# Optimization experiments

Measured on AMD Instinct MI355X. Metric: run time of the kernel, lower is better.

## Reference

```python
import jax, jax.numpy as jnp
import numpy as np
from itertools import combinations

NUM_FIELDS = 32
EMB = 64
# static pair index lists for combinations(range(NUM_FIELDS), 2)
_PAIRS = np.array(list(combinations(range(NUM_FIELDS), 2)), dtype=np.int32)  # (496, 2)
I_IDX = jnp.asarray(_PAIRS[:, 0])
J_IDX = jnp.asarray(_PAIRS[:, 1])


def bilinear_each(feats, W):
    # feats: (B, F, E); W: (F-1, E, E) with torch Linear convention y = x @ W[i].T
    # transform fields 0..F-2 with their own weight
    t = jnp.einsum('bfe,foe->bfo', feats[:, :NUM_FIELDS - 1, :], W)  # (B, F-1, E)
    # pair (i, j): t[:, i] * feats[:, j]
    return t[:, I_IDX, :] * feats[:, J_IDX, :]  # (B, P, E)


def se_block(x, se_w1, se_w2):
    # x: (B, F, E)
    Z = jnp.mean(x, axis=-1)                      # (B, F)
    A = jax.nn.relu(Z @ se_w1.T)                  # (B, F//r)
    A = jax.nn.sigmoid(A @ se_w2.T)               # (B, F)
    return x * A[:, :, None]


def setup_inputs() -> dict:
    key = jax.random.key(0)
    ks = jax.random.split(key, 12)
    B, F, E = 1024, NUM_FIELDS, EMB
    P = F * (F - 1) // 2
    d_in = 2 * P * E  # 63488
    h1, h2, nc = 1024, 512, 1
    red = max(1, F // 8)
    s = lambda *sh: 1.0 / np.sqrt(sh[-1])
    inp = {
        'x': jax.random.normal(ks[0], (B, F, E), dtype=jnp.float32),
        'W_bil1': jax.random.normal(ks[1], (F - 1, E, E), jnp.float32) * s(E),
        'W_bil2': jax.random.normal(ks[2], (F - 1, E, E), jnp.float32) * s(E),
        'se_w1': jax.random.normal(ks[3], (red, F), jnp.float32) * s(F),
        'se_w2': jax.random.normal(ks[4], (F, red), jnp.float32) * s(red),
        'fc0_w': jax.random.normal(ks[5], (h1, d_in), jnp.float32) * s(d_in),
        'fc0_b': jnp.zeros((h1,), jnp.float32),
        'fc1_w': jax.random.normal(ks[6], (h2, h1), jnp.float32) * s(h1),
        'fc1_b': jnp.zeros((h2,), jnp.float32),
        'fc2_w': jax.random.normal(ks[7], (nc, h2), jnp.float32) * s(h2),
        'fc2_b': jnp.zeros((nc,), jnp.float32),
    }
    return inp


def reference(x, W_bil1, W_bil2, se_w1, se_w2, fc0_w, fc0_b, fc1_w, fc1_b, fc2_w, fc2_b):
    f1 = bilinear_each(x, W_bil1)                    # (B, P, E)
    f2 = bilinear_each(se_block(x, se_w1, se_w2), W_bil2)  # (B, P, E)
    feat = jnp.concatenate([f1, f2], axis=1).reshape(x.shape[0], -1)  # (B, 2*P*E)
    h = jax.nn.relu(feat @ fc0_w.T + fc0_b)
    h = jax.nn.relu(h @ fc1_w.T + fc1_b)
    y = jax.nn.sigmoid(h @ fc2_w.T + fc2_b)
    return y
```

## Files before the change

kernel.cpp:

```cpp
#include <hip/hip_runtime.h>
#include <hip/hip_bf16.h>
#include <stdint.h>


typedef __attribute__((ext_vector_type(4))) int   int4v;
typedef __attribute__((ext_vector_type(4))) unsigned uint4v;
typedef __attribute__((ext_vector_type(4))) float f32x4;

__device__ __forceinline__ unsigned short f32_bf16(float f) {
  unsigned u = __builtin_bit_cast(unsigned, f);
  u = (u + 0x7fffu + ((u >> 16) & 1u)) >> 16;
  return (unsigned short)u;
}
__device__ __forceinline__ unsigned pk_bf16(float lo, float hi) {
  return (unsigned)f32_bf16(lo) | ((unsigned)f32_bf16(hi) << 16);
}
__device__ __forceinline__ unsigned cvt_pk(float lo, float hi) {
  unsigned r;
  asm("v_cvt_pk_bf16_f32 %0, %1, %2" : "=v"(r) : "v"(lo), "v"(hi));
  return r;
}

__global__ __launch_bounds__(256) void se_kernel(
    const float* __restrict__ x, const float* __restrict__ w1,
    const float* __restrict__ w2, float* __restrict__ scale) {
  __shared__ float Z[32];
  __shared__ float A1[4];
  int b = blockIdx.x;
  int t = threadIdx.x;
  int f = t >> 3, sub = t & 7;
  const float4* xp = (const float4*)(x + (size_t)b * 2048 + f * 64 + sub * 8);
  float4 v0 = xp[0], v1 = xp[1];
  float s = v0.x + v0.y + v0.z + v0.w + v1.x + v1.y + v1.z + v1.w;
  s += __shfl_down(s, 4, 8);
  s += __shfl_down(s, 2, 8);
  s += __shfl_down(s, 1, 8);
  if (sub == 0) Z[f] = s * (1.0f / 64.0f);
  __syncthreads();
  if (t < 4) {
    float a = 0.f;
#pragma unroll
    for (int ff = 0; ff < 32; ++ff) a += Z[ff] * w1[t * 32 + ff];
    A1[t] = fmaxf(a, 0.f);
  }
  __syncthreads();
  if (t < 32) {
    float a = 0.f;
#pragma unroll
    for (int r = 0; r < 4; ++r) a += A1[r] * w2[t * 4 + r];
    scale[b * 32 + t] = 1.f / (1.f + expf(-a));
  }
}

__global__ __launch_bounds__(256) void t_kernel(
    const float* __restrict__ x, const float* __restrict__ W1,
    const float* __restrict__ W2, const float* __restrict__ scale,
    float* __restrict__ t1, float* __restrict__ t2) {
  __shared__ float Wl[64 * 65];
  __shared__ float xs[64 * 65];
  int f = blockIdx.x;
  int b0 = blockIdx.y * 64;
  int which = blockIdx.z;
  const float* W = (which ? W2 : W1) + (size_t)f * 4096;
  float* tout = which ? t2 : t1;
  int t = threadIdx.x;
#pragma unroll
  for (int it = 0; it < 16; ++it) {
    int idx = it * 256 + t;
    int o = idx >> 6, e = idx & 63;
    Wl[o * 65 + e] = W[idx];
  }
#pragma unroll
  for (int it = 0; it < 16; ++it) {
    int idx = it * 256 + t;
    int bl = idx >> 6, e = idx & 63;
    float v = x[(size_t)(b0 + bl) * 2048 + f * 64 + e];
    if (which) v *= scale[(b0 + bl) * 32 + f];
    xs[bl * 65 + e] = v;
  }
  __syncthreads();
  int o = t & 63, g = t >> 6;
  float sum[16];
#pragma unroll
  for (int r = 0; r < 16; ++r) sum[r] = 0.f;
#pragma unroll 4
  for (int e = 0; e < 64; ++e) {
    float wv = Wl[o * 65 + e];
#pragma unroll
    for (int r = 0; r < 16; ++r) sum[r] += xs[(g * 16 + r) * 65 + e] * wv;
  }
#pragma unroll
  for (int r = 0; r < 16; ++r)
    tout[(size_t)(b0 + g * 16 + r) * 1984 + f * 64 + o] = sum[r];
}

__global__ __launch_bounds__(256) void feat_kernel(
    const float* __restrict__ x, const float* __restrict__ t1,
    const float* __restrict__ t2, const float* __restrict__ scale,
    unsigned short* __restrict__ feat) {
  int gid = blockIdx.x * 256 + threadIdx.x;
  int b = gid / 7936;
  int rem = gid - b * 7936;
  int s = rem >> 3;
  int e0 = (rem & 7) * 8;
  int which = (s >= 496) ? 1 : 0;
  int p = s - (which ? 496 : 0);
  int i = (int)((63.0f - sqrtf((float)(3969 - 8 * p))) * 0.5f);
  while ((i * (63 - i)) / 2 > p) --i;
  while (((i + 1) * (62 - i)) / 2 <= p) ++i;
  int j = i + 1 + (p - (i * (63 - i)) / 2);
  const float* tp = (which ? t2 : t1) + (size_t)b * 1984 + i * 64 + e0;
  const float* xp = x + (size_t)b * 2048 + j * 64 + e0;
  float sc = which ? scale[b * 32 + j] : 1.0f;
  float4 ta = *(const float4*)tp, tb = *(const float4*)(tp + 4);
  float4 xa = *(const float4*)xp, xb = *(const float4*)(xp + 4);
  uint4v o;
  o.x = pk_bf16(ta.x * xa.x * sc, ta.y * xa.y * sc);
  o.y = pk_bf16(ta.z * xa.z * sc, ta.w * xa.w * sc);
  o.z = pk_bf16(tb.x * xb.x * sc, tb.y * xb.y * sc);
  o.w = pk_bf16(tb.z * xb.z * sc, tb.w * xb.w * sc);
  *(uint4v*)(feat + (size_t)b * 63488 + s * 64 + e0) = o;
}

__device__ __forceinline__ void mfma_bf16(f32x4& d, int4v a, int4v b) {
  asm volatile("v_mfma_f32_16x16x32_bf16 %0, %1, %2, %0"
               : "+v"(d) : "v"(a), "v"(b));
}

#define FBM 256
#define FBN 256
#define FBK 64

__device__ __forceinline__ void fc0_phase(
    const unsigned short* sAb, const unsigned short* sBb,
    int kk, int wr, int wc, int l15, int l4, f32x4 (&acc)[8][4]) {
  int4v av[8], bv[4];
#pragma unroll
  for (int i = 0; i < 8; ++i) {
    int ar = wr + i * 16 + l15;
    av[i] = *(const int4v*)&sAb[(ar * 8 + ((kk * 4 + l4) ^ (ar & 7))) * 8];
  }
#pragma unroll
  for (int j = 0; j < 4; ++j) {
    int br = wc + j * 16 + l15;
    bv[j] = *(const int4v*)&sBb[(br * 8 + ((kk * 4 + l4) ^ (br & 7))) * 8];
  }
  __builtin_amdgcn_s_setprio(1);
#pragma unroll
  for (int i = 0; i < 8; ++i)
#pragma unroll
    for (int j = 0; j < 4; ++j) mfma_bf16(acc[i][j], av[i], bv[j]);
  __builtin_amdgcn_s_setprio(0);
}

__global__ __launch_bounds__(512, 2) void gemm_fc0(
    const unsigned short* __restrict__ A, const float* __restrict__ Bp,
    float* __restrict__ Cp, int M, int N, int K, int kz) {
  __shared__ unsigned short sA[2][FBM * FBK];
  __shared__ unsigned short sB[2][FBN * FBK];
  int tid = threadIdx.x;
  int lane = tid & 63;
  int wave = tid >> 6;
  int bid = blockIdx.x;
  int m0 = (bid >> 6) << 8;
  int s  = bid & 63;
  int n0 = (s & 3) << 8;
  int z  = s >> 2;
  int wr = (wave >> 2) * 128, wc = (wave & 3) * 64;
  int l15 = lane & 15, l4 = lane >> 4;
  int kbase = z * kz;
  int nt = kz / FBK;

  f32x4 acc[8][4];
#pragma unroll
  for (int i = 0; i < 8; ++i)
#pragma unroll
    for (int j = 0; j < 4; ++j) acc[i][j] = (f32x4){0.f, 0.f, 0.f, 0.f};

  unsigned aOff[4]; int aDst[4];
  unsigned bOff[4]; int bDst[4];
#pragma unroll
  for (int it = 0; it < 4; ++it) {
    int c = it * 512 + tid;
    int r = c >> 3, l = c & 7;
    aOff[it] = (unsigned)(m0 + r) * (unsigned)K + (unsigned)((l ^ (r & 7)) << 3);
    aDst[it] = c * 8;
    bOff[it] = (unsigned)(n0 + r) * (unsigned)K + (unsigned)(l << 3);
    bDst[it] = (r * 8 + (l ^ (r & 7))) * 8;
  }

#define FC0_STAGE_A(buf, kt)                                                   \
  _Pragma("unroll") for (int it = 0; it < 4; ++it) {                           \
    __builtin_amdgcn_global_load_lds(                                          \
        (const __attribute__((address_space(1))) void*)(A + aOff[it] + (kt)),  \
        (__attribute__((address_space(3))) void*)(&sA[buf][aDst[it]]), 16, 0, 0); \
  }
#define FC0_LOAD_B(kt)                                                         \
  _Pragma("unroll") for (int it = 0; it < 4; ++it) {                           \
    const float* gp = Bp + bOff[it] + (kt);                                    \
    bst[2 * it]     = *(const float4*)gp;                                      \
    bst[2 * it + 1] = *(const float4*)(gp + 4);                                \
  }
#define FC0_WRITE_B(buf)                                                       \
  _Pragma("unroll") for (int it = 0; it < 4; ++it) {                           \
    uint4v q;                                                                  \
    q.x = cvt_pk(bst[2 * it].x, bst[2 * it].y);                                \
    q.y = cvt_pk(bst[2 * it].z, bst[2 * it].w);                                \
    q.z = cvt_pk(bst[2 * it + 1].x, bst[2 * it + 1].y);                        \
    q.w = cvt_pk(bst[2 * it + 1].z, bst[2 * it + 1].w);                        \
    *(uint4v*)(&sB[buf][bDst[it]]) = q;                                        \
  }

  float4 bst[8];
  FC0_LOAD_B(kbase)
  FC0_WRITE_B(0)
  FC0_STAGE_A(0, kbase)
  FC0_LOAD_B(kbase + FBK)
  __builtin_amdgcn_sched_barrier(0);
  asm volatile("s_waitcnt vmcnt(8) lgkmcnt(0)" ::: "memory");
  __builtin_amdgcn_sched_barrier(0);
  __builtin_amdgcn_s_barrier();
  __builtin_amdgcn_sched_barrier(0);

  for (int t = 0; t < nt; ++t) {
    int cur = t & 1, nxt = cur ^ 1;
    if (t + 1 < nt) { FC0_STAGE_A(nxt, kbase + (t + 1) * FBK) }
    __builtin_amdgcn_sched_barrier(0);
    fc0_phase(sA[cur], sB[cur], 0, wr, wc, l15, l4, acc);
    __builtin_amdgcn_sched_barrier(0);
    if (t + 1 < nt) {
      asm volatile("s_waitcnt vmcnt(4)" ::: "memory");
      __builtin_amdgcn_sched_barrier(0);
      FC0_WRITE_B(nxt)
    }
    __builtin_amdgcn_sched_barrier(0);
    if (t + 2 < nt) { FC0_LOAD_B(kbase + (t + 2) * FBK) }
    __builtin_amdgcn_sched_barrier(0);
    fc0_phase(sA[cur], sB[cur], 1, wr, wc, l15, l4, acc);
    __builtin_amdgcn_sched_barrier(0);
    if (t + 2 < nt) {
      asm volatile("s_waitcnt vmcnt(8) lgkmcnt(0)" ::: "memory");
    } else {
      asm volatile("s_waitcnt vmcnt(0) lgkmcnt(0)" ::: "memory");
    }
    __builtin_amdgcn_sched_barrier(0);
    __builtin_amdgcn_s_barrier();
    __builtin_amdgcn_sched_barrier(0);
  }
#undef FC0_STAGE_A
#undef FC0_LOAD_B
#undef FC0_WRITE_B

  asm volatile("s_nop 7\n\ts_nop 7\n\ts_nop 7" ::: "memory");
  float* cp = Cp + (size_t)z * M * N;
#pragma unroll
  for (int i = 0; i < 8; ++i) {
    int rbase = m0 + wr + i * 16 + l4 * 4;
#pragma unroll
    for (int j = 0; j < 4; ++j) {
      int cc = n0 + wc + j * 16 + l15;
#pragma unroll
      for (int r = 0; r < 4; ++r)
        cp[(size_t)(rbase + r) * N + cc] = acc[i][j][r];
    }
  }
}

#define BM 256
#define BN 128
#define BK 64

__global__ __launch_bounds__(256, 2) void gemm_bt(
    const unsigned short* __restrict__ A, const float* __restrict__ B,
    float* __restrict__ Cp, int M, int N, int K, int kz) {
  __shared__ unsigned short sA[BM * BK];
  __shared__ unsigned short sB[BN * BK];
  int tid = threadIdx.x;
  int lane = tid & 63, wave = tid >> 6;
  int n0 = blockIdx.x * BN, m0 = blockIdx.y * BM;
  int z = blockIdx.z;
  int wr = (wave >> 1) * 128, wc = (wave & 1) * 64;
  int l15 = lane & 15, l4 = lane >> 4;
  f32x4 acc[8][4];
#pragma unroll
  for (int i = 0; i < 8; ++i)
#pragma unroll
    for (int j = 0; j < 4; ++j) acc[i][j] = (f32x4){0.f, 0.f, 0.f, 0.f};

  int kend = z * kz + kz;
  for (int kt = z * kz; kt < kend; kt += BK) {
#pragma unroll
    for (int it = 0; it < 8; ++it) {
      int c = it * 256 + tid;
      int r = c >> 3, p = c & 7;
      int gcol = (p ^ (r & 7)) * 8;
      const unsigned short* gp = A + (size_t)(m0 + r) * K + kt + gcol;
      __builtin_amdgcn_global_load_lds(
          (const __attribute__((address_space(1))) void*)gp,
          (__attribute__((address_space(3))) void*)(&sA[c * 8]), 16, 0, 0);
    }
#pragma unroll
    for (int it = 0; it < 4; ++it) {
      int c = it * 256 + tid;
      int r = c >> 3, l = c & 7;
      const float* gp = B + (size_t)(n0 + r) * K + kt + l * 8;
      float4 f0 = *(const float4*)gp;
      float4 f1 = *(const float4*)(gp + 4);
      uint4v q;
      q.x = pk_bf16(f0.x, f0.y); q.y = pk_bf16(f0.z, f0.w);
      q.z = pk_bf16(f1.x, f1.y); q.w = pk_bf16(f1.z, f1.w);
      int p = l ^ (r & 7);
      *(uint4v*)(&sB[(r * 8 + p) * 8]) = q;
    }
    __syncthreads();
#pragma unroll
    for (int kk = 0; kk < 2; ++kk) {
      int lc = kk * 4 + l4;
      int4v av[8], bv[4];
#pragma unroll
      for (int i = 0; i < 8; ++i) {
        int ar = wr + i * 16 + l15;
        av[i] = *(const int4v*)&sA[(ar * 8 + (lc ^ (ar & 7))) * 8];
      }
#pragma unroll
      for (int j = 0; j < 4; ++j) {
        int br = wc + j * 16 + l15;
        bv[j] = *(const int4v*)&sB[(br * 8 + (lc ^ (br & 7))) * 8];
      }
#pragma unroll
      for (int i = 0; i < 8; ++i)
#pragma unroll
        for (int j = 0; j < 4; ++j) mfma_bf16(acc[i][j], av[i], bv[j]);
    }
    __syncthreads();
  }
  asm volatile("s_nop 7\n\ts_nop 7\n\ts_nop 7" ::: "memory");
  float* cp = Cp + (size_t)z * M * N;
#pragma unroll
  for (int i = 0; i < 8; ++i) {
    int rbase = m0 + wr + i * 16 + l4 * 4;
#pragma unroll
    for (int j = 0; j < 4; ++j) {
      int cc = n0 + wc + j * 16 + l15;
#pragma unroll
      for (int r = 0; r < 4; ++r)
        cp[(size_t)(rbase + r) * N + cc] = acc[i][j][r];
    }
  }
}

__global__ __launch_bounds__(256) void reduce_bias_act(
    const float* __restrict__ parts, const float* __restrict__ bias,
    int MN, int nmask, int nz, unsigned short* __restrict__ out_bf,
    float* __restrict__ out_f) {
  int idx = blockIdx.x * 256 + threadIdx.x;
  if (idx >= MN) return;
  float s = 0.f;
  for (int z = 0; z < nz; ++z) s += parts[(size_t)z * MN + idx];
  s += bias[idx & nmask];
  s = fmaxf(s, 0.f);
  if (out_bf) out_bf[idx] = f32_bf16(s);
  else out_f[idx] = s;
}

__global__ __launch_bounds__(256) void fc2_kernel(
    const float* __restrict__ h2, const float* __restrict__ w,
    const float* __restrict__ b, float* __restrict__ out) {
  int wave = threadIdx.x >> 6, lane = threadIdx.x & 63;
  int row = blockIdx.x * 4 + wave;
  const float4* hp = (const float4*)(h2 + (size_t)row * 512);
  const float4* wp = (const float4*)w;
  int i0 = lane * 2;
  float4 a0 = hp[i0], a1 = hp[i0 + 1];
  float4 w0 = wp[i0], w1 = wp[i0 + 1];
  float s = a0.x * w0.x + a0.y * w0.y + a0.z * w0.z + a0.w * w0.w +
            a1.x * w1.x + a1.y * w1.y + a1.z * w1.z + a1.w * w1.w;
#pragma unroll
  for (int off = 32; off > 0; off >>= 1) s += __shfl_down(s, off);
  if (lane == 0) out[row] = 1.f / (1.f + expf(-(s + b[0])));
}

extern "C" void kernel_launch(void* const* d_in, const int* in_sizes, int n_in,
                              void* d_out, int out_size, void* d_ws, size_t ws_size,
                              hipStream_t stream) {
  const float* x     = (const float*)d_in[0];
  const float* Wb1   = (const float*)d_in[1];
  const float* Wb2   = (const float*)d_in[2];
  const float* se_w1 = (const float*)d_in[3];
  const float* se_w2 = (const float*)d_in[4];
  const float* fc0_w = (const float*)d_in[5];
  const float* fc0_b = (const float*)d_in[6];
  const float* fc1_w = (const float*)d_in[7];
  const float* fc1_b = (const float*)d_in[8];
  const float* fc2_w = (const float*)d_in[9];
  const float* fc2_b = (const float*)d_in[10];
  (void)in_sizes; (void)n_in; (void)out_size; (void)ws_size;

  char* ws = (char*)d_ws;
  float*          scale = (float*)(ws + 0);
  float*          t1    = (float*)(ws + 131072);
  float*          t2    = (float*)(ws + 8257536);
  unsigned short* feat  = (unsigned short*)(ws + 16384000);
  float*          hp    = (float*)(ws + 146407424);
  unsigned short* h1b   = (unsigned short*)(ws + 213516288);
  float*          h2    = (float*)(ws + 215613440);
  float*          out   = (float*)d_out;

  se_kernel<<<1024, 256, 0, stream>>>(x, se_w1, se_w2, scale);
  t_kernel<<<dim3(31, 16, 2), 256, 0, stream>>>(x, Wb1, Wb2, scale, t1, t2);
  feat_kernel<<<31744, 256, 0, stream>>>(x, t1, t2, scale, feat);
  gemm_fc0<<<256, 512, 0, stream>>>(feat, fc0_w, hp, 1024, 1024, 63488, 3968);
  reduce_bias_act<<<4096, 256, 0, stream>>>(hp, fc0_b, 1024 * 1024, 1023, 16, h1b, nullptr);
  gemm_bt<<<dim3(4, 4, 16), 256, 0, stream>>>(h1b, fc1_w, hp, 1024, 512, 1024, 64);
  reduce_bias_act<<<2048, 256, 0, stream>>>(hp, fc1_b, 1024 * 512, 511, 16, nullptr, h2);
  fc2_kernel<<<256, 256, 0, stream>>>(h2, fc2_w, fc2_b, out);
}
```

Measured before the change: 555.2 us.

## Split fc0 main loop into ping-pong sub-phases with barrier-interleaved LDS reads

Restructures the fc0 GEMM K-loop into four sub-phases per tile, each reading a 2-column slice of B fragments from LDS, then barrier-synchronising before an 8x2 MFMA burst, in a ping-pong style across the two waves per SIMD. LDS buffers are swapped by pointer, and the last two tiles are peeled so the loop body carries no conditionals. The aim is to overlap LDS reads and global loads of one wave group with MFMA of the other and to cut register pressure from B fragments. It adds many more workgroup barriers per tile, which may stall if the phases are not balanced.

```diff
diff --git a/kernel.cpp b/kernel.cpp
--- a/kernel.cpp
+++ b/kernel.cpp
@@ -131,25 +131,30 @@
 #define FBN 256
 #define FBK 64
 
-__device__ __forceinline__ void fc0_phase(
-    const unsigned short* sAb, const unsigned short* sBb,
-    int kk, int wr, int wc, int l15, int l4, f32x4 (&acc)[8][4]) {
-  int4v av[8], bv[4];
+__device__ __forceinline__ void fc0_read_av(
+    const unsigned short* sAb, int kk, int wr, int l15, int l4, int4v (&av)[8]) {
 #pragma unroll
   for (int i = 0; i < 8; ++i) {
     int ar = wr + i * 16 + l15;
     av[i] = *(const int4v*)&sAb[(ar * 8 + ((kk * 4 + l4) ^ (ar & 7))) * 8];
   }
-#pragma unroll
-  for (int j = 0; j < 4; ++j) {
-    int br = wc + j * 16 + l15;
+}
+__device__ __forceinline__ void fc0_read_bv(
+    const unsigned short* sBb, int kk, int j0, int wc, int l15, int l4,
+    int4v (&bv)[2]) {
+#pragma unroll
+  for (int j = 0; j < 2; ++j) {
+    int br = wc + (j0 + j) * 16 + l15;
     bv[j] = *(const int4v*)&sBb[(br * 8 + ((kk * 4 + l4) ^ (br & 7))) * 8];
   }
+}
+__device__ __forceinline__ void fc0_mfma8x2(
+    f32x4 (&acc)[8][4], int j0, int4v (&av)[8], int4v (&bv)[2]) {
   __builtin_amdgcn_s_setprio(1);
 #pragma unroll
   for (int i = 0; i < 8; ++i)
 #pragma unroll
-    for (int j = 0; j < 4; ++j) mfma_bf16(acc[i][j], av[i], bv[j]);
+    for (int j = 0; j < 2; ++j) mfma_bf16(acc[i][j0 + j], av[i], bv[j]);
   __builtin_amdgcn_s_setprio(0);
 }
 
@@ -189,11 +194,16 @@
     bDst[it] = (r * 8 + (l ^ (r & 7))) * 8;
   }
 
-#define FC0_STAGE_A(buf, kt)                                                   \
+  unsigned short* sAc = &sA[0][0];
+  unsigned short* sAn = &sA[1][0];
+  unsigned short* sBc = &sB[0][0];
+  unsigned short* sBn = &sB[1][0];
+
+#define FC0_STAGE_A(dstp, kt)                                                  \
   _Pragma("unroll") for (int it = 0; it < 4; ++it) {                           \
     __builtin_amdgcn_global_load_lds(                                          \
         (const __attribute__((address_space(1))) void*)(A + aOff[it] + (kt)),  \
-        (__attribute__((address_space(3))) void*)(&sA[buf][aDst[it]]), 16, 0, 0); \
+        (__attribute__((address_space(3))) void*)((dstp) + aDst[it]), 16, 0, 0); \
   }
 #define FC0_LOAD_B(kt)                                                         \
   _Pragma("unroll") for (int it = 0; it < 4; ++it) {                           \
@@ -201,55 +211,81 @@
     bst[2 * it]     = *(const float4*)gp;                                      \
     bst[2 * it + 1] = *(const float4*)(gp + 4);                                \
   }
-#define FC0_WRITE_B(buf)                                                       \
+#define FC0_WRITE_B(dstp)                                                      \
   _Pragma("unroll") for (int it = 0; it < 4; ++it) {                           \
     uint4v q;                                                                  \
     q.x = cvt_pk(bst[2 * it].x, bst[2 * it].y);                                \
     q.y = cvt_pk(bst[2 * it].z, bst[2 * it].w);                                \
     q.z = cvt_pk(bst[2 * it + 1].x, bst[2 * it + 1].y);                        \
     q.w = cvt_pk(bst[2 * it + 1].z, bst[2 * it + 1].w);                        \
-    *(uint4v*)(&sB[buf][bDst[it]]) = q;                                        \
-  }
+    *(uint4v*)((dstp) + bDst[it]) = q;                                         \
+  }
+#define BAR()  __builtin_amdgcn_s_barrier()
+#define LGKM0() asm volatile("s_waitcnt lgkmcnt(0)" ::: "memory")
+
+#define FC0_TILE(KT1, KT2, DO_SA, DO_LB, WAITS)                                \
+  {                                                                            \
+                                      \
+    if (DO_SA) { FC0_STAGE_A(sAn, KT1) }                                       \
+    fc0_read_av(sAc, 0, wr, l15, l4, av);                                      \
+    fc0_read_bv(sBc, 0, 0, wc, l15, l4, bv);                                   \
+    BAR(); LGKM0();                                                            \
+    fc0_mfma8x2(acc, 0, av, bv);                                               \
+    BAR();                                                                     \
+              \
+    if (DO_SA) {                                                               \
+      asm volatile("s_waitcnt vmcnt(4)" ::: "memory");                         \
+      FC0_WRITE_B(sBn)                                                         \
+    }                                                                          \
+    fc0_read_bv(sBc, 0, 2, wc, l15, l4, bv);                                   \
+    BAR(); LGKM0();                                                            \
+    fc0_mfma8x2(acc, 2, av, bv);                                               \
+    BAR();                                                                     \
+                                 \
+    if (DO_LB) { FC0_LOAD_B(KT2) }                                             \
+    fc0_read_av(sAc, 1, wr, l15, l4, av);                                      \
+    fc0_read_bv(sBc, 1, 0, wc, l15, l4, bv);                                   \
+    BAR(); LGKM0();                                                            \
+    fc0_mfma8x2(acc, 0, av, bv);                                               \
+    BAR();                                                                     \
+                           \
+    fc0_read_bv(sBc, 1, 2, wc, l15, l4, bv);                                   \
+    BAR(); LGKM0();                                                            \
+    fc0_mfma8x2(acc, 2, av, bv);                                               \
+    asm volatile("s_waitcnt " WAITS ::: "memory");                             \
+    BAR();                                                                     \
+  }
+#define FC0_SWAP()                                                             \
+  { unsigned short* tp;                                                        \
+    tp = sAc; sAc = sAn; sAn = tp;                                             \
+    tp = sBc; sBc = sBn; sBn = tp; }
 
   float4 bst[8];
+  int4v av[8], bv[2];
   FC0_LOAD_B(kbase)
-  FC0_WRITE_B(0)
-  FC0_STAGE_A(0, kbase)
+  FC0_STAGE_A(sAc, kbase)
+  asm volatile("s_waitcnt vmcnt(4)" ::: "memory");
+  FC0_WRITE_B(sBc)
   FC0_LOAD_B(kbase + FBK)
-  __builtin_amdgcn_sched_barrier(0);
   asm volatile("s_waitcnt vmcnt(8) lgkmcnt(0)" ::: "memory");
-  __builtin_amdgcn_sched_barrier(0);
-  __builtin_amdgcn_s_barrier();
-  __builtin_amdgcn_sched_barrier(0);
-
-  for (int t = 0; t < nt; ++t) {
-    int cur = t & 1, nxt = cur ^ 1;
-    if (t + 1 < nt) { FC0_STAGE_A(nxt, kbase + (t + 1) * FBK) }
-    __builtin_amdgcn_sched_barrier(0);
-    fc0_phase(sA[cur], sB[cur], 0, wr, wc, l15, l4, acc);
-    __builtin_amdgcn_sched_barrier(0);
-    if (t + 1 < nt) {
-      asm volatile("s_waitcnt vmcnt(4)" ::: "memory");
-      __builtin_amdgcn_sched_barrier(0);
-      FC0_WRITE_B(nxt)
-    }
-    __builtin_amdgcn_sched_barrier(0);
-    if (t + 2 < nt) { FC0_LOAD_B(kbase + (t + 2) * FBK) }
-    __builtin_amdgcn_sched_barrier(0);
-    fc0_phase(sA[cur], sB[cur], 1, wr, wc, l15, l4, acc);
-    __builtin_amdgcn_sched_barrier(0);
-    if (t + 2 < nt) {
-      asm volatile("s_waitcnt vmcnt(8) lgkmcnt(0)" ::: "memory");
-    } else {
-      asm volatile("s_waitcnt vmcnt(0) lgkmcnt(0)" ::: "memory");
-    }
-    __builtin_amdgcn_sched_barrier(0);
-    __builtin_amdgcn_s_barrier();
-    __builtin_amdgcn_sched_barrier(0);
-  }
+  BAR();
+
+#pragma unroll 2
+  for (int t = 0; t < nt - 2; ++t) {
+    FC0_TILE(kbase + (t + 1) * FBK, kbase + (t + 2) * FBK, 1, 1, "vmcnt(8)")
+    FC0_SWAP()
+  }
+  FC0_TILE(kbase + (nt - 1) * FBK, 0, 1, 0, "vmcnt(0)")
+  FC0_SWAP()
+  FC0_TILE(0, 0, 0, 0, "vmcnt(0)")
+
+#undef FC0_TILE
+#undef FC0_SWAP
 #undef FC0_STAGE_A
 #undef FC0_LOAD_B
 #undef FC0_WRITE_B
+#undef BAR
+#undef LGKM0
 
   asm volatile("s_nop 7\n\ts_nop 7\n\ts_nop 7" ::: "memory");
   float* cp = Cp + (size_t)z * M * N;
```

Measured after the change: 578.6 us. 4.2% more time.
